# Performance work log

Hardware: AMD Instinct MI355X
Metric: run time of the kernel (lower is better)

## Reference

```python
import jax, jax.numpy as jnp
import numpy as np
import math

EPS = 1e-5      # artanh boundary clamp (Poincare ball)
MIN_NORM = 1e-15

def _norm(x):
    return jnp.clip(jnp.linalg.norm(x, axis=-1, keepdims=True), MIN_NORM, None)

def artanh(x):
    x = jnp.clip(x, -1.0 + EPS, 1.0 - EPS)
    return 0.5 * (jnp.log1p(x) - jnp.log1p(-x))

def expmap0(u):
    # c = 1 Poincare ball: tanh(||u||) * u / ||u||
    n = _norm(u)
    return jnp.tanh(n) * u / n

def mobius_matvec(M, x):
    # geoopt: mx = x @ M^T; res = tanh(||mx||/||x|| * artanh(||x||)) * mx/||mx||
    xn = _norm(x)
    mx = x @ M.T
    mxn = _norm(mx)
    res = jnp.tanh(mxn / xn * artanh(xn)) * mx / mxn
    zero_row = jnp.all(mx == 0, axis=-1, keepdims=True)
    return jnp.where(zero_row, jnp.zeros_like(res), res)

def mobius_add(x, y):
    x2 = jnp.sum(x * x, axis=-1, keepdims=True)
    y2 = jnp.sum(y * y, axis=-1, keepdims=True)
    xy = jnp.sum(x * y, axis=-1, keepdims=True)
    num = (1.0 + 2.0 * xy + y2) * x + (1.0 - x2) * y
    den = 1.0 + 2.0 * xy + x2 * y2
    return num / jnp.clip(den, MIN_NORM, None)

def dist(x, y):
    # d(x,y) = 2 * artanh(|| (-x) mobius+ y ||); reduces the last dim
    return 2.0 * artanh(_norm(mobius_add(-x, y)))[..., 0]

def setup_inputs() -> dict:
    key = jax.random.key(0)
    k1, k2, k3, k4, k5 = jax.random.split(key, 5)
    B, S, H, D = 64, 1024, 768, 64
    bound = 1.0 / math.sqrt(D)
    sequence_output = jax.random.normal(k1, (B, S, H), dtype=jnp.float32) * 0.1
    proj = jax.random.uniform(k2, (H, D), dtype=jnp.float32, minval=-0.05, maxval=0.05)
    trans = jax.random.uniform(k3, (D, D), dtype=jnp.float32, minval=-0.05, maxval=0.05)
    pos = expmap0(jax.random.uniform(k4, (D,), dtype=jnp.float32, minval=-bound, maxval=bound))
    neg = expmap0(jax.random.uniform(k5, (D,), dtype=jnp.float32, minval=-bound, maxval=bound))
    return {"sequence_output": sequence_output, "proj": proj, "trans": trans,
            "pos": pos, "neg": neg}

def reference(sequence_output, proj, trans, pos, neg):
    t = sequence_output @ proj          # [B, S, 64]
    t = expmap0(t)
    t = mobius_matvec(trans, t)
    pos_logits = dist(neg, t).sum(-1)   # [B]
    neg_logits = dist(pos, t).sum(-1)   # [B]
    return jnp.stack((neg_logits, pos_logits), axis=-1)  # [B, 2]
```

## Files before the change

kernel.cpp:

```cpp
#include <hip/hip_runtime.h>
#include <math.h>

#define MIN_NORM 1e-15f
#define BOUND_EPS 1e-5f

typedef __attribute__((ext_vector_type(8))) short short8v;
typedef __attribute__((ext_vector_type(4))) float f32x4;

__device__ __forceinline__ unsigned short f2bf(float f) {
  unsigned int u = __float_as_uint(f);
  unsigned int r = (u + 0x7FFFu + ((u >> 16) & 1u)) >> 16;
  return (unsigned short)r;
}
__device__ __forceinline__ unsigned int pack2bf(float a, float b) {
  return (unsigned int)f2bf(a) | ((unsigned int)f2bf(b) << 16);
}

__device__ __forceinline__ float gred16(float v) {
  v += __shfl_xor(v, 1, 64);
  v += __shfl_xor(v, 2, 64);
  v += __shfl_xor(v, 4, 64);
  v += __shfl_xor(v, 8, 64);
  return v;
}
__device__ __forceinline__ float wred64(float v) {
#pragma unroll
  for (int off = 32; off; off >>= 1) v += __shfl_xor(v, off, 64);
  return v;
}
__device__ __forceinline__ float artanh_c(float x) {
  x = fminf(fmaxf(x, -1.f + BOUND_EPS), 1.f - BOUND_EPS);
  return 0.5f * logf((1.f + x) / (1.f - x));
}

__global__ __launch_bounds__(256) void poincare_prep(
    const float* __restrict__ proj, const float* __restrict__ trans,
    unsigned short* __restrict__ projB, unsigned short* __restrict__ transB) {
  int idx = blockIdx.x * 256 + threadIdx.x;
  if (idx < 49152) {
    int k = idx >> 6, d = idx & 63;
    int kt = k >> 5, t5 = k & 31, lk = t5 >> 3, j = t5 & 7;
    int nt = d >> 4, lr = d & 15;
    int l = lk * 16 + lr;
    projB[((kt * 4 + nt) * 64 + l) * 8 + j] = f2bf(proj[idx]);
  } else if (idx < 49152 + 4096) {
    int i2 = idx - 49152;
    int r = i2 >> 6, c = i2 & 63;
    int nt = r >> 4, lr = r & 15;
    int kt = c >> 5, lk = (c >> 3) & 3, j = c & 7;
    int l = lk * 16 + lr;
    transB[((kt * 4 + nt) * 64 + l) * 8 + j] = f2bf(trans[i2]);
  }
}

__global__ __launch_bounds__(256, 3) void poincare_main(
    const float* __restrict__ seq,
    const unsigned short* __restrict__ projB,
    const unsigned short* __restrict__ transB,
    const float* __restrict__ pos, const float* __restrict__ neg,
    float* __restrict__ wsPart) {
  __shared__ unsigned short As[2][64][136];
  __shared__ unsigned short teL[4][16 * 64];
  __shared__ float partial[4][2];

  const int tid = threadIdx.x;
  const int w = tid >> 6, l = tid & 63;
  const int lr = l & 15, lk = l >> 4;
  const long bIdx = blockIdx.x;
  const float* sBase = seq + bIdx * 64 * 768;

  const int rS = tid >> 5;
  const int cS = (tid & 31) * 4;

  f32x4 acc[4];
#pragma unroll
  for (int nt = 0; nt < 4; ++nt) acc[nt] = (f32x4){0.f, 0.f, 0.f, 0.f};

#pragma unroll
  for (int i = 0; i < 8; ++i) {
    int r = i * 8 + rS;
    float4 v = *(const float4*)(sBase + r * 768 + cS);
    *(uint2*)&As[0][r][cS] = make_uint2(pack2bf(v.x, v.y), pack2bf(v.z, v.w));
  }
  __syncthreads();

#pragma unroll 2
  for (int ch = 0; ch < 6; ++ch) {
    const int cur = ch & 1;

    short8v bf[4][4];
#pragma unroll
    for (int ktl = 0; ktl < 4; ++ktl) {
      const unsigned short* pb = projB + (ch * 4 + ktl) * 2048 + l * 8;
      bf[ktl][0] = *(const short8v*)(pb);
      bf[ktl][1] = *(const short8v*)(pb + 512);
      bf[ktl][2] = *(const short8v*)(pb + 1024);
      bf[ktl][3] = *(const short8v*)(pb + 1536);
    }

    float4 st[8];
    if (ch < 5) {
#pragma unroll
      for (int i = 0; i < 8; ++i) {
        int r = i * 8 + rS;
        st[i] = *(const float4*)(sBase + r * 768 + (ch + 1) * 128 + cS);
      }
    }

#pragma unroll
    for (int ktl = 0; ktl < 4; ++ktl) {
      short8v av = *(const short8v*)&As[cur][w * 16 + lr][ktl * 32 + lk * 8];
      acc[0] = __builtin_amdgcn_mfma_f32_16x16x32_bf16(av, bf[ktl][0], acc[0], 0, 0, 0);
      acc[1] = __builtin_amdgcn_mfma_f32_16x16x32_bf16(av, bf[ktl][1], acc[1], 0, 0, 0);
      acc[2] = __builtin_amdgcn_mfma_f32_16x16x32_bf16(av, bf[ktl][2], acc[2], 0, 0, 0);
      acc[3] = __builtin_amdgcn_mfma_f32_16x16x32_bf16(av, bf[ktl][3], acc[3], 0, 0, 0);
    }

    if (ch < 5) {
#pragma unroll
      for (int i = 0; i < 8; ++i) {
        int r = i * 8 + rS;
        *(uint2*)&As[cur ^ 1][r][cS] =
            make_uint2(pack2bf(st[i].x, st[i].y), pack2bf(st[i].z, st[i].w));
      }
    }
    __syncthreads();
  }

  float th[4];
#pragma unroll
  for (int i = 0; i < 4; ++i) {
    float s = acc[0][i] * acc[0][i] + acc[1][i] * acc[1][i] +
              acc[2][i] * acc[2][i] + acc[3][i] * acc[3][i];
    s = gred16(s);
    float n = fmaxf(sqrtf(s), MIN_NORM);
    float t = tanhf(n);
    th[i] = fmaxf(t, MIN_NORM);
    float sc = t / n;
#pragma unroll
    for (int nt = 0; nt < 4; ++nt) acc[nt][i] *= sc;
  }

  unsigned short* buf = teL[w];
#pragma unroll
  for (int i = 0; i < 4; ++i) {
    int row = lk * 4 + i;
    int sw = (row & 7) << 3;
#pragma unroll
    for (int nt = 0; nt < 4; ++nt) {
      int col = nt * 16 + lr;
      buf[row * 64 + (col ^ sw)] = f2bf(acc[nt][i]);
    }
  }
  __syncthreads();

  f32x4 acc2[4];
#pragma unroll
  for (int nt = 0; nt < 4; ++nt) acc2[nt] = (f32x4){0.f, 0.f, 0.f, 0.f};
  const unsigned short* pT = transB + l * 8;
#pragma unroll
  for (int kt = 0; kt < 2; ++kt) {
    short8v a2 = *(const short8v*)&buf[lr * 64 + ((kt * 32 + lk * 8) ^ ((lr & 7) << 3))];
    const unsigned short* pt = pT + kt * 2048;
    short8v c0 = *(const short8v*)(pt);
    short8v c1 = *(const short8v*)(pt + 512);
    short8v c2 = *(const short8v*)(pt + 1024);
    short8v c3 = *(const short8v*)(pt + 1536);
    acc2[0] = __builtin_amdgcn_mfma_f32_16x16x32_bf16(a2, c0, acc2[0], 0, 0, 0);
    acc2[1] = __builtin_amdgcn_mfma_f32_16x16x32_bf16(a2, c1, acc2[1], 0, 0, 0);
    acc2[2] = __builtin_amdgcn_mfma_f32_16x16x32_bf16(a2, c2, acc2[2], 0, 0, 0);
    acc2[3] = __builtin_amdgcn_mfma_f32_16x16x32_bf16(a2, c3, acc2[3], 0, 0, 0);
  }

  float xp[4], xq[4];
#pragma unroll
  for (int nt = 0; nt < 4; ++nt) {
    xp[nt] = pos[nt * 16 + lr];
    xq[nt] = neg[nt * 16 + lr];
  }
  float x2p = wred64(xp[0] * xp[0] + xp[1] * xp[1] + xp[2] * xp[2] + xp[3] * xp[3]) * 0.25f;
  float x2n = wred64(xq[0] * xq[0] + xq[1] * xq[1] + xq[2] * xq[2] + xq[3] * xq[3]) * 0.25f;

  float distP = 0.f, distN = 0.f;
#pragma unroll
  for (int i = 0; i < 4; ++i) {
    float m0 = acc2[0][i], m1 = acc2[1][i], m2 = acc2[2][i], m3 = acc2[3][i];
    float s = gred16(m0 * m0 + m1 * m1 + m2 * m2 + m3 * m3);
    float mxn = fmaxf(sqrtf(s), MIN_NORM);
    float xn = th[i];
    float rs = tanhf(mxn / xn * artanh_c(xn)) / mxn;
    float r0 = rs * m0, r1 = rs * m1, r2 = rs * m2, r3 = rs * m3;
    float y2 = gred16(r0 * r0 + r1 * r1 + r2 * r2 + r3 * r3);
    float xyP = -gred16(xp[0] * r0 + xp[1] * r1 + xp[2] * r2 + xp[3] * r3);
    float xyN = -gred16(xq[0] * r0 + xq[1] * r1 + xq[2] * r2 + xq[3] * r3);
    {
      float A = 1.f + 2.f * xyP + y2, B = 1.f - x2p;
      float inv = 1.f / fmaxf(1.f + 2.f * xyP + x2p * y2, MIN_NORM);
      float v0 = (B * r0 - A * xp[0]) * inv, v1 = (B * r1 - A * xp[1]) * inv;
      float v2 = (B * r2 - A * xp[2]) * inv, v3 = (B * r3 - A * xp[3]) * inv;
      float nv = fmaxf(sqrtf(gred16(v0 * v0 + v1 * v1 + v2 * v2 + v3 * v3)), MIN_NORM);
      distP += 2.f * artanh_c(nv);
    }
    {
      float A = 1.f + 2.f * xyN + y2, B = 1.f - x2n;
      float inv = 1.f / fmaxf(1.f + 2.f * xyN + x2n * y2, MIN_NORM);
      float v0 = (B * r0 - A * xq[0]) * inv, v1 = (B * r1 - A * xq[1]) * inv;
      float v2 = (B * r2 - A * xq[2]) * inv, v3 = (B * r3 - A * xq[3]) * inv;
      float nv = fmaxf(sqrtf(gred16(v0 * v0 + v1 * v1 + v2 * v2 + v3 * v3)), MIN_NORM);
      distN += 2.f * artanh_c(nv);
    }
  }
  float tP = wred64(distP) * 0.0625f;
  float tN = wred64(distN) * 0.0625f;
  if (l == 0) { partial[w][0] = tP; partial[w][1] = tN; }
  __syncthreads();
  if (tid == 0) {
    wsPart[bIdx * 2 + 0] = partial[0][0] + partial[1][0] + partial[2][0] + partial[3][0];
    wsPart[bIdx * 2 + 1] = partial[0][1] + partial[1][1] + partial[2][1] + partial[3][1];
  }
}

__global__ __launch_bounds__(128) void poincare_reduce(const float* __restrict__ wsPart,
                                                       float* __restrict__ out) {
  int t = threadIdx.x;
  int b = t >> 1, j = t & 1;
  float s = 0.f;
#pragma unroll
  for (int i = 0; i < 16; ++i) s += wsPart[(b * 16 + i) * 2 + j];
  out[b * 2 + j] = s;
}

extern "C" void kernel_launch(void* const* d_in, const int* in_sizes, int n_in,
                              void* d_out, int out_size, void* d_ws, size_t ws_size,
                              hipStream_t stream) {
  const float* seq = (const float*)d_in[0];
  const float* proj = (const float*)d_in[1];
  const float* trans = (const float*)d_in[2];
  const float* pos = (const float*)d_in[3];
  const float* neg = (const float*)d_in[4];

  unsigned short* projB = (unsigned short*)d_ws;
  unsigned short* transB = projB + 49152;
  float* wsPart = (float*)((char*)d_ws + 106496);
  float* out = (float*)d_out;

  poincare_prep<<<208, 256, 0, stream>>>(proj, trans, projB, transB);
  poincare_main<<<1024, 256, 0, stream>>>(seq, projB, transB, pos, neg, wsPart);
  poincare_reduce<<<1, 128, 0, stream>>>(wsPart, out);
}
```

Baseline: 51.21 us.

## Restructure projection GEMM to split N across waves with full-row staging

The first GEMM now works on one 16-row slab at a time. Each slab stages all 768 columns of 16 rows into LDS as bf16, and each wave computes one 16-column N tile over the full K, rather than each wave owning 16 rows and all four N tiles. Results are transposed back through an LDS float buffer so the rest of the epilogue is unchanged. This cuts per-wave register use, since only one accumulator and one B fragment are live at a time, and the launch bound occupancy target rises from 3 to 4. In exchange, the double-buffered prefetch that overlapped global loads with MFMA is gone, and each slab now needs extra syncs.

```diff
diff --git a/kernel.cpp b/kernel.cpp
--- a/kernel.cpp
+++ b/kernel.cpp
@@ -53,79 +53,68 @@
   }
 }
 
-__global__ __launch_bounds__(256, 3) void poincare_main(
+__global__ __launch_bounds__(256, 4) void poincare_main(
     const float* __restrict__ seq,
     const unsigned short* __restrict__ projB,
     const unsigned short* __restrict__ transB,
     const float* __restrict__ pos, const float* __restrict__ neg,
     float* __restrict__ wsPart) {
-  __shared__ unsigned short As[2][64][136];
-  __shared__ unsigned short teL[4][16 * 64];
+  __shared__ unsigned short stageS[16][776];
+  __shared__ unsigned short teL[4][1024];
   __shared__ float partial[4][2];
 
   const int tid = threadIdx.x;
   const int w = tid >> 6, l = tid & 63;
   const int lr = l & 15, lk = l >> 4;
   const long bIdx = blockIdx.x;
-  const float* sBase = seq + bIdx * 64 * 768;
-
-  const int rS = tid >> 5;
-  const int cS = (tid & 31) * 4;
+
+  f32x4 acc4[4];
+#pragma unroll
+  for (int m = 0; m < 4; ++m) acc4[m] = (f32x4){0.f, 0.f, 0.f, 0.f};
+
+#pragma unroll
+  for (int m = 0; m < 4; ++m) {
+    const float* cBase = seq + (bIdx * 64 + m * 16) * 768;
+
+    float4 st[12];
+#pragma unroll
+    for (int r = 0; r < 4; ++r)
+#pragma unroll
+      for (int c3 = 0; c3 < 3; ++c3)
+        st[r * 3 + c3] = *(const float4*)(cBase + (w * 4 + r) * 768 + c3 * 256 + l * 4);
+#pragma unroll
+    for (int r = 0; r < 4; ++r)
+#pragma unroll
+      for (int c3 = 0; c3 < 3; ++c3) {
+        float4 v = st[r * 3 + c3];
+        *(uint2*)&stageS[w * 4 + r][c3 * 256 + l * 4] =
+            make_uint2(pack2bf(v.x, v.y), pack2bf(v.z, v.w));
+      }
+    __syncthreads();
+
+#pragma unroll
+    for (int kt = 0; kt < 24; ++kt) {
+      short8v bfr = *(const short8v*)(projB + (kt * 4 + w) * 512 + l * 8);
+      short8v av = *(const short8v*)&stageS[lr][kt * 32 + lk * 8];
+      acc4[m] = __builtin_amdgcn_mfma_f32_16x16x32_bf16(av, bfr, acc4[m], 0, 0, 0);
+    }
+    __syncthreads();
+  }
+
+  float* tF = (float*)&stageS[0][0];
+#pragma unroll
+  for (int m = 0; m < 4; ++m)
+#pragma unroll
+    for (int i = 0; i < 4; ++i)
+      tF[(m * 16 + lk * 4 + i) * 68 + (w * 16 + lr)] = acc4[m][i];
+  __syncthreads();
 
   f32x4 acc[4];
 #pragma unroll
-  for (int nt = 0; nt < 4; ++nt) acc[nt] = (f32x4){0.f, 0.f, 0.f, 0.f};
-
-#pragma unroll
-  for (int i = 0; i < 8; ++i) {
-    int r = i * 8 + rS;
-    float4 v = *(const float4*)(sBase + r * 768 + cS);
-    *(uint2*)&As[0][r][cS] = make_uint2(pack2bf(v.x, v.y), pack2bf(v.z, v.w));
-  }
-  __syncthreads();
-
-#pragma unroll 2
-  for (int ch = 0; ch < 6; ++ch) {
-    const int cur = ch & 1;
-
-    short8v bf[4][4];
-#pragma unroll
-    for (int ktl = 0; ktl < 4; ++ktl) {
-      const unsigned short* pb = projB + (ch * 4 + ktl) * 2048 + l * 8;
-      bf[ktl][0] = *(const short8v*)(pb);
-      bf[ktl][1] = *(const short8v*)(pb + 512);
-      bf[ktl][2] = *(const short8v*)(pb + 1024);
-      bf[ktl][3] = *(const short8v*)(pb + 1536);
-    }
-
-    float4 st[8];
-    if (ch < 5) {
-#pragma unroll
-      for (int i = 0; i < 8; ++i) {
-        int r = i * 8 + rS;
-        st[i] = *(const float4*)(sBase + r * 768 + (ch + 1) * 128 + cS);
-      }
-    }
-
-#pragma unroll
-    for (int ktl = 0; ktl < 4; ++ktl) {
-      short8v av = *(const short8v*)&As[cur][w * 16 + lr][ktl * 32 + lk * 8];
-      acc[0] = __builtin_amdgcn_mfma_f32_16x16x32_bf16(av, bf[ktl][0], acc[0], 0, 0, 0);
-      acc[1] = __builtin_amdgcn_mfma_f32_16x16x32_bf16(av, bf[ktl][1], acc[1], 0, 0, 0);
-      acc[2] = __builtin_amdgcn_mfma_f32_16x16x32_bf16(av, bf[ktl][2], acc[2], 0, 0, 0);
-      acc[3] = __builtin_amdgcn_mfma_f32_16x16x32_bf16(av, bf[ktl][3], acc[3], 0, 0, 0);
-    }
-
-    if (ch < 5) {
-#pragma unroll
-      for (int i = 0; i < 8; ++i) {
-        int r = i * 8 + rS;
-        *(uint2*)&As[cur ^ 1][r][cS] =
-            make_uint2(pack2bf(st[i].x, st[i].y), pack2bf(st[i].z, st[i].w));
-      }
-    }
-    __syncthreads();
-  }
+  for (int nt = 0; nt < 4; ++nt)
+#pragma unroll
+    for (int i = 0; i < 4; ++i)
+      acc[nt][i] = tF[(w * 16 + lk * 4 + i) * 68 + (nt * 16 + lr)];
 
   float th[4];
 #pragma unroll
```

After: 70.14 us. +37.0%, slower.
